# Optimization experiments

Hardware: AMD Instinct MI355X
Metric: run time of the kernel (lower is better)

The kernel has to match this reference:

```python
import jax, jax.numpy as jnp
import numpy as np

N = 100000
E = 1600000
D = 128


def setup_inputs() -> dict:
    key = jax.random.key(0)
    ks = jax.random.split(key, 9)
    s = 1.0 / np.sqrt(D)
    return {
        "x": jax.random.normal(ks[0], (N, D), dtype=jnp.float32),
        "edge_index": jax.random.randint(ks[1], (2, E), 0, N, dtype=jnp.int64),
        # SAGEConv layer 1: lin_l (neighbor path, with bias), lin_r (root path, no bias)
        "Wl1": jax.random.normal(ks[2], (D, D), dtype=jnp.float32) * s,
        "bl1": jnp.zeros((D,), dtype=jnp.float32),
        "Wr1": jax.random.normal(ks[3], (D, D), dtype=jnp.float32) * s,
        # SAGEConv layer 2
        "Wl2": jax.random.normal(ks[4], (D, D), dtype=jnp.float32) * s,
        "bl2": jnp.zeros((D,), dtype=jnp.float32),
        "Wr2": jax.random.normal(ks[5], (D, D), dtype=jnp.float32) * s,
    }


def _sage_conv(x, src, dst, Wl, bl, Wr):
    # PyG SAGEConv, aggr='mean', root_weight=True:
    #   out = lin_l(mean_{j in N(i)} x_j) + lin_r(x_i)
    msg = x[src]                                              # [E, D] gather
    agg = jax.ops.segment_sum(msg, dst, num_segments=N)       # [N, D]
    cnt = jax.ops.segment_sum(jnp.ones((src.shape[0],), x.dtype), dst, num_segments=N)
    agg = agg / jnp.maximum(cnt, 1.0)[:, None]                # mean aggregation
    return agg @ Wl.T + bl + x @ Wr.T


def reference(x, edge_index, Wl1, bl1, Wr1, Wl2, bl2, Wr2):
    src, dst = edge_index[0], edge_index[1]
    h = jax.nn.relu(_sage_conv(x, src, dst, Wl1, bl1, Wr1))
    out = _sage_conv(h, src, dst, Wl2, bl2, Wr2)
    return out
```

## Files before the change

### kernel.cpp

```cpp
#include <hip/hip_runtime.h>
#include <stdint.h>

#define DN 128
#define NBITS 6
#define BNODES 64
#define HB 2048
#define NSL 64
#define NLOC 256

__host__ __device__ static inline int divup(int a, int b){ return (a+b-1)/b; }

typedef __attribute__((ext_vector_type(8))) short bf16x8;
typedef __attribute__((ext_vector_type(4))) float floatx4;

__device__ __forceinline__ unsigned short f2bf(float f){
  unsigned int x = __float_as_uint(f);
  unsigned int r = x + 0x7fffu + ((x >> 16) & 1u);
  return (unsigned short)(r >> 16);
}
__device__ __forceinline__ unsigned int pack2(unsigned short a, unsigned short b){
  return (unsigned int)a | ((unsigned int)b << 16);
}


__global__ __launch_bounds__(256)
void hist_pass(const int* __restrict__ dst, int* __restrict__ gHist, int E){
  __shared__ int h[NLOC];
  int p = blockIdx.x & 7, s = blockIdx.x >> 3;
  int t = threadIdx.x;
  h[t] = 0;
  __syncthreads();
  int n4 = E >> 2, per4 = divup(n4, NSL);
  int lo = s*per4, hi = min(lo+per4, n4);
  const int4* dst4 = (const int4*)dst;
  for (int i = lo + t; i < hi; i += 256){
    int4 d4 = dst4[i];
    int dd[4] = {d4.x, d4.y, d4.z, d4.w};
    #pragma unroll
    for (int j=0;j<4;j++){
      int b = dd[j] >> NBITS;
      if ((b & 7) == p) atomicAdd(&h[b>>3], 1);
    }
  }
  if (s == NSL-1){
    for (int e = (n4<<2) + t; e < E; e += 256){
      int b = dst[e] >> NBITS;
      if ((b & 7) == p) atomicAdd(&h[b>>3], 1);
    }
  }
  __syncthreads();
  gHist[blockIdx.x*NLOC + t] = h[t];
}

__global__ __launch_bounds__(256)
void scan_offsets(const int* __restrict__ gHist, int* __restrict__ blockOffset,
                  int* __restrict__ bucketTotal){
  int b = blockIdx.x*4 + (threadIdx.x >> 6);
  int k = threadIdx.x & 63;
  int p = b & 7, lb = b >> 3;
  int idx = (k*8 + p)*NLOC + lb;
  int v = gHist[idx];
  int sft = v;
  #pragma unroll
  for (int off=1; off<64; off<<=1){
    int u = __shfl_up(sft, off, 64);
    if (k >= off) sft += u;
  }
  blockOffset[idx] = sft - v;
  if (k == 63) bucketTotal[b] = sft;
}

__global__ __launch_bounds__(256)
void bucket_base(const int* __restrict__ bucketTotal, int* __restrict__ bucketBase){
  __shared__ int s[256];
  int t = threadIdx.x;
  int v[8]; int sum = 0;
  #pragma unroll
  for (int j=0;j<8;j++){ v[j] = bucketTotal[t*8+j]; sum += v[j]; }
  s[t] = sum; __syncthreads();
  for (int off=1; off<256; off<<=1){
    int y = (t>=off)? s[t-off] : 0;
    __syncthreads();
    s[t] += y;
    __syncthreads();
  }
  int excl = s[t] - sum;
  #pragma unroll
  for (int j=0;j<8;j++){ bucketBase[t*8+j] = excl; excl += v[j]; }
  if (t == 255) bucketBase[HB] = excl;
}

__global__ __launch_bounds__(256)
void scatter_pass(const int* __restrict__ src, const int* __restrict__ dst,
                  const int* __restrict__ bucketBase, const int* __restrict__ blockOffset,
                  unsigned int* __restrict__ packed, int E){
  __shared__ int cur[NLOC];
  int p = blockIdx.x & 7, s = blockIdx.x >> 3;
  int t = threadIdx.x;
  cur[t] = bucketBase[(t<<3)|p] + blockOffset[blockIdx.x*NLOC + t];
  __syncthreads();
  int n4 = E >> 2, per4 = divup(n4, NSL);
  int lo = s*per4, hi = min(lo+per4, n4);
  const int4* dst4 = (const int4*)dst;
  const int4* src4 = (const int4*)src;
  for (int i = lo + t; i < hi; i += 256){
    int4 d4 = dst4[i];
    int4 s4 = src4[i];
    int dd[4] = {d4.x, d4.y, d4.z, d4.w};
    int ss[4] = {s4.x, s4.y, s4.z, s4.w};
    #pragma unroll
    for (int j=0;j<4;j++){
      int d = dd[j], b = d >> NBITS;
      if ((b & 7) == p){
        int pos = atomicAdd(&cur[b>>3], 1);
        packed[pos] = (unsigned)ss[j] | ((unsigned)(d & (BNODES-1)) << 17);
      }
    }
  }
  if (s == NSL-1){
    for (int e = (n4<<2) + t; e < E; e += 256){
      int d = dst[e], b = d >> NBITS;
      if ((b & 7) == p){
        int pos = atomicAdd(&cur[b>>3], 1);
        packed[pos] = (unsigned)src[e] | ((unsigned)(d & (BNODES-1)) << 17);
      }
    }
  }
}

__global__ __launch_bounds__(256)
void node_sort(const int* __restrict__ bucketBase, const unsigned int* __restrict__ packed,
               int* __restrict__ csr_src, int* __restrict__ nodeOff, int n){
  __shared__ int cnts[BNODES], offs[BNODES+1], cursor[BNODES];
  int b = blockIdx.x, t = threadIdx.x;
  int beg = bucketBase[b], end = bucketBase[b+1], cnt = end - beg;
  if (t < BNODES) cnts[t] = 0;
  __syncthreads();
  for (int i=t; i<cnt; i+=256) atomicAdd(&cnts[(packed[beg+i]>>17)&63], 1);
  __syncthreads();
  if (t < BNODES){
    int v = cnts[t], sft = v;
    #pragma unroll
    for (int off=1; off<64; off<<=1){
      int u = __shfl_up(sft, off, 64);
      if (t >= off) sft += u;
    }
    offs[t] = sft - v; cursor[t] = sft - v;
    if (t == 63) offs[BNODES] = sft;
  }
  __syncthreads();
  for (int i=t; i<cnt; i+=256){
    unsigned pk = packed[beg+i];
    int nd = (pk>>17)&63;
    int r = atomicAdd(&cursor[nd], 1);
    csr_src[beg + r] = (int)(pk & 0x1FFFFu);
  }
  if (t <= BNODES){
    int node = b*BNODES + t;
    if (node <= n) nodeOff[node] = beg + offs[t];
  }
}


__global__ __launch_bounds__(256)
void convert_x_kernel(const float* __restrict__ src, unsigned short* __restrict__ dst, int count8){
  int i = blockIdx.x*256 + threadIdx.x;
  if (i >= count8) return;
  const float4* s = (const float4*)src + (size_t)i*2;
  float4 a = s[0], b = s[1];
  uint4 o;
  o.x = pack2(f2bf(a.x), f2bf(a.y));
  o.y = pack2(f2bf(a.z), f2bf(a.w));
  o.z = pack2(f2bf(b.x), f2bf(b.y));
  o.w = pack2(f2bf(b.z), f2bf(b.w));
  ((uint4*)dst)[i] = o;
}

__global__ __launch_bounds__(256)
void convert_w_kernel(const float* __restrict__ w0, const float* __restrict__ w1,
                      const float* __restrict__ w2, const float* __restrict__ w3,
                      unsigned short* __restrict__ dst){
  int tid = blockIdx.x*256 + threadIdx.x;
  if (tid >= 8192) return;
  int mat = tid >> 11, off = tid & 2047;
  const float* w = (mat==0)?w0:(mat==1)?w1:(mat==2)?w2:w3;
  const float4* s = (const float4*)w + (size_t)off*2;
  float4 a = s[0], b = s[1];
  uint4 o;
  o.x = pack2(f2bf(a.x), f2bf(a.y));
  o.y = pack2(f2bf(a.z), f2bf(a.w));
  o.z = pack2(f2bf(b.x), f2bf(b.y));
  o.w = pack2(f2bf(b.z), f2bf(b.w));
  ((uint4*)(dst + (size_t)mat*16384))[off] = o;
}

__global__ __launch_bounds__(256)
void aggregate_csr(const unsigned short* __restrict__ xb, const int* __restrict__ nodeOff,
                   const int* __restrict__ csr_src, unsigned short* __restrict__ aggb, int n){
  int g = (blockIdx.x*256 + threadIdx.x) >> 6;
  if (g >= n) return;
  int lane = threadIdx.x & 63;
  int j = lane >> 4;
  int l = lane & 15;
  int beg = nodeOff[g], end = nodeOff[g+1];
  float acc[8] = {0,0,0,0,0,0,0,0};
  #define ACCUM(u) { unsigned int w;                                   \
      w=(u).x; acc[0]+=__uint_as_float(w<<16); acc[1]+=__uint_as_float(w&0xffff0000u); \
      w=(u).y; acc[2]+=__uint_as_float(w<<16); acc[3]+=__uint_as_float(w&0xffff0000u); \
      w=(u).z; acc[4]+=__uint_as_float(w<<16); acc[5]+=__uint_as_float(w&0xffff0000u); \
      w=(u).w; acc[6]+=__uint_as_float(w<<16); acc[7]+=__uint_as_float(w&0xffff0000u); }
  const uint4* x4 = (const uint4*)xb;
  int p = beg;
  for (; p + 8 <= end; p += 8){
    int s0 = csr_src[p + j];
    int s1 = csr_src[p + 4 + j];
    uint4 u0 = x4[(size_t)s0*16 + l];
    uint4 u1 = x4[(size_t)s1*16 + l];
    ACCUM(u0) ACCUM(u1)
  }
  for (; p + 4 <= end; p += 4){
    int s0 = csr_src[p + j];
    uint4 u0 = x4[(size_t)s0*16 + l];
    ACCUM(u0)
  }
  int rem = end - p;
  if (j < rem){
    int s0 = csr_src[p + j];
    uint4 u0 = x4[(size_t)s0*16 + l];
    ACCUM(u0)
  }
  #undef ACCUM
  #pragma unroll
  for (int k=0;k<8;k++){
    acc[k] += __shfl_xor(acc[k], 16, 64);
    acc[k] += __shfl_xor(acc[k], 32, 64);
  }
  if (j == 0){
    float inv = 1.f / fmaxf((float)(end-beg), 1.f);
    uint4 o;
    o.x = pack2(f2bf(acc[0]*inv), f2bf(acc[1]*inv));
    o.y = pack2(f2bf(acc[2]*inv), f2bf(acc[3]*inv));
    o.z = pack2(f2bf(acc[4]*inv), f2bf(acc[5]*inv));
    o.w = pack2(f2bf(acc[6]*inv), f2bf(acc[7]*inv));
    ((uint4*)(aggb + (size_t)g*DN))[l] = o;
  }
}

template<bool RELU, bool OUT_BF16>
__global__ __launch_bounds__(256)
void gemm_mfma(const unsigned short* __restrict__ A1, const unsigned short* __restrict__ W1b,
               const unsigned short* __restrict__ A2, const unsigned short* __restrict__ W2b,
               const float* __restrict__ bias, void* __restrict__ out,
               int rt_total, int rt_per_block)
{
  int wave = threadIdx.x >> 6;
  int lane = threadIdx.x & 63;
  int m = lane & 15, quad = lane >> 4;

  bf16x8 Bf[2][2][4];
  {
    const unsigned short* Ws[2] = {W1b, W2b};
    #pragma unroll
    for (int c2=0;c2<2;c2++){
      int col = wave*32 + c2*16 + m;
      #pragma unroll
      for (int mat=0;mat<2;mat++){
        const unsigned short* wrow = Ws[mat] + (size_t)col*DN + quad*8;
        #pragma unroll
        for (int kc=0;kc<4;kc++)
          Bf[c2][mat][kc] = *(const bf16x8*)(wrow + kc*32);
      }
    }
  }
  float bv0 = bias[wave*32 + m];
  float bv1 = bias[wave*32 + 16 + m];

  int rt_begin = blockIdx.x * rt_per_block;
  int rt_end = rt_begin + rt_per_block; if (rt_end > rt_total) rt_end = rt_total;

  for (int rt = rt_begin; rt < rt_end; ++rt){
    const unsigned short* a1p = A1 + ((size_t)(rt*16 + m))*DN + quad*8;
    const unsigned short* a2p = A2 + ((size_t)(rt*16 + m))*DN + quad*8;
    bf16x8 Af[2][4];
    #pragma unroll
    for (int kc=0;kc<4;kc++){
      Af[0][kc] = *(const bf16x8*)(a1p + kc*32);
      Af[1][kc] = *(const bf16x8*)(a2p + kc*32);
    }
    __syncthreads();
    floatx4 acc0 = {0.f,0.f,0.f,0.f}, acc1 = {0.f,0.f,0.f,0.f};
    #pragma unroll
    for (int mat=0; mat<2; mat++)
      #pragma unroll
      for (int kc=0; kc<4; kc++){
        acc0 = __builtin_amdgcn_mfma_f32_16x16x32_bf16(Af[mat][kc], Bf[0][mat][kc], acc0, 0,0,0);
        acc1 = __builtin_amdgcn_mfma_f32_16x16x32_bf16(Af[mat][kc], Bf[1][mat][kc], acc1, 0,0,0);
      }
    #pragma unroll
    for (int r=0;r<4;r++){
      int row = rt*16 + quad*4 + r;
      float v0 = acc0[r] + bv0;
      float v1 = acc1[r] + bv1;
      if (RELU){ v0 = fmaxf(v0, 0.f); v1 = fmaxf(v1, 0.f); }
      if (OUT_BF16){
        unsigned short* o = (unsigned short*)out + (size_t)row*DN + wave*32 + m;
        o[0]  = f2bf(v0);
        o[16] = f2bf(v1);
      } else {
        float* o = (float*)out + (size_t)row*DN + wave*32 + m;
        o[0]  = v0;
        o[16] = v1;
      }
    }
  }
}


extern "C" void kernel_launch(void* const* d_in, const int* in_sizes, int n_in,
                              void* d_out, int out_size, void* d_ws, size_t ws_size,
                              hipStream_t stream) {
  const float* x   = (const float*)d_in[0];
  const int*   ei  = (const int*)d_in[1];
  const float* Wl1 = (const float*)d_in[2];
  const float* bl1 = (const float*)d_in[3];
  const float* Wr1 = (const float*)d_in[4];
  const float* Wl2 = (const float*)d_in[5];
  const float* bl2 = (const float*)d_in[6];
  const float* Wr2 = (const float*)d_in[7];

  const int n = in_sizes[0] / DN;
  const int E = in_sizes[1] / 2;
  const int* src = ei;
  const int* dst = ei + E;

  char* ws = (char*)d_ws;
  char* ws_end = ws + ws_size;
  int* gHist       = (int*)ws;  ws += (size_t)NSL*8*NLOC*4;
  int* blockOffset = (int*)ws;  ws += (size_t)NSL*8*NLOC*4;
  int* bucketTotal = (int*)ws;  ws += (size_t)HB*4;
  int* bucketBase  = (int*)ws;  ws += (size_t)(HB+1)*4;
  ws = (char*)(((uintptr_t)ws + 255) & ~(uintptr_t)255);
  unsigned int* packed = (unsigned int*)ws; ws += (size_t)E*4;
  int* csr_src     = (int*)ws;  ws += (size_t)E*4;
  int* nodeOff     = (int*)ws;  ws += (size_t)(n+1)*4;
  ws = (char*)(((uintptr_t)ws + 255) & ~(uintptr_t)255);
  unsigned short* Wb   = (unsigned short*)ws; ws += 4*16384*2;
  unsigned short* xb   = (unsigned short*)ws; ws += (size_t)n*DN*2;
  unsigned short* aggb = (unsigned short*)ws; ws += (size_t)n*DN*2;
  unsigned short* hb = xb;
  if (ws + (size_t)n*DN*2 <= ws_end) { hb = (unsigned short*)ws; ws += (size_t)n*DN*2; }

  unsigned short* Wl1b = Wb;
  unsigned short* Wr1b = Wb + 16384;
  unsigned short* Wl2b = Wb + 2*16384;
  unsigned short* Wr2b = Wb + 3*16384;

  hist_pass   <<<NSL*8, 256,0,stream>>>(dst, gHist, E);
  scan_offsets<<<HB/4,  256,0,stream>>>(gHist, blockOffset, bucketTotal);
  bucket_base <<<1,     256,0,stream>>>(bucketTotal, bucketBase);
  scatter_pass<<<NSL*8, 256,0,stream>>>(src, dst, bucketBase, blockOffset, packed, E);
  node_sort   <<<HB,    256,0,stream>>>(bucketBase, packed, csr_src, nodeOff, n);

  convert_x_kernel<<<divup(n*DN/8,256),256,0,stream>>>(x, xb, n*DN/8);
  convert_w_kernel<<<32,256,0,stream>>>(Wl1, Wr1, Wl2, Wr2, Wb);

  const int rt_total = n / 16;
  const int rt_per_block = 5;
  const int gblocks = divup(rt_total, rt_per_block);
  const int agrid = divup(n*64, 256);

  aggregate_csr<<<agrid,256,0,stream>>>(xb, nodeOff, csr_src, aggb, n);
  gemm_mfma<true, true><<<gblocks,256,0,stream>>>(aggb, Wl1b, xb, Wr1b, bl1, hb, rt_total, rt_per_block);
  aggregate_csr<<<agrid,256,0,stream>>>(hb, nodeOff, csr_src, aggb, n);
  gemm_mfma<false,false><<<gblocks,256,0,stream>>>(aggb, Wl2b, hb, Wr2b, bl2, d_out, rt_total, rt_per_block);
}
```

Baseline: 365.0 us.

## Fuse mean aggregation and dual GEMM into one SAGE layer kernel

Adds a fused kernel per SAGE layer: each block gathers and mean-aggregates 32 nodes into shared memory as bf16, then runs MFMA against both Wl and Wr with bias and optional ReLU in the epilogue. This removes the round trip of the aggregated buffer through global memory and halves the per-layer kernel launches. In exchange, each block reloads both weight matrices into registers for only 32 rows, and the gather phase uses 16 lanes per node, which may cut memory-level parallelism compared with the separate aggregate kernel. The old path is kept as a fallback when the workspace cannot hold a separate h buffer.

```diff
diff --git a/kernel.cpp b/kernel.cpp
--- a/kernel.cpp
+++ b/kernel.cpp
@@ -193,6 +193,130 @@
   o.w = pack2(f2bf(b.z), f2bf(b.w));
   ((uint4*)(dst + (size_t)mat*16384))[off] = o;
 }
+
+template<bool RELU, bool OUT_BF16>
+__global__ __launch_bounds__(256, 4)
+void fused_sage(const unsigned short* __restrict__ xin, const int* __restrict__ nodeOff,
+                const int* __restrict__ csr_src,
+                const unsigned short* __restrict__ Wlb, const unsigned short* __restrict__ Wrb,
+                const float* __restrict__ bias, void* __restrict__ out, int n)
+{
+  __shared__ uint4 Asm[32][16];
+  int t = threadIdx.x;
+  int tile = blockIdx.x;
+  int nl = t >> 4;
+  int l  = t & 15;
+  const uint4* x4 = (const uint4*)xin;
+
+  #pragma unroll
+  for (int half = 0; half < 2; ++half){
+    int node_local = nl + half*16;
+    int g = tile*32 + node_local;
+    float acc[8] = {0,0,0,0,0,0,0,0};
+    int deg = 0;
+    if (g < n){
+      int beg = nodeOff[g], end = nodeOff[g+1];
+      deg = end - beg;
+      #define ACCUM(u) { unsigned int w;                                   \
+          w=(u).x; acc[0]+=__uint_as_float(w<<16); acc[1]+=__uint_as_float(w&0xffff0000u); \
+          w=(u).y; acc[2]+=__uint_as_float(w<<16); acc[3]+=__uint_as_float(w&0xffff0000u); \
+          w=(u).z; acc[4]+=__uint_as_float(w<<16); acc[5]+=__uint_as_float(w&0xffff0000u); \
+          w=(u).w; acc[6]+=__uint_as_float(w<<16); acc[7]+=__uint_as_float(w&0xffff0000u); }
+      int p = beg;
+      for (; p+4 <= end; p += 4){
+        int s0 = csr_src[p], s1 = csr_src[p+1], s2 = csr_src[p+2], s3 = csr_src[p+3];
+        uint4 u0 = x4[(size_t)s0*16 + l];
+        uint4 u1 = x4[(size_t)s1*16 + l];
+        uint4 u2 = x4[(size_t)s2*16 + l];
+        uint4 u3 = x4[(size_t)s3*16 + l];
+        ACCUM(u0) ACCUM(u1) ACCUM(u2) ACCUM(u3)
+      }
+      for (; p < end; ++p){
+        int s0 = csr_src[p];
+        uint4 u0 = x4[(size_t)s0*16 + l];
+        ACCUM(u0)
+      }
+      #undef ACCUM
+    }
+    float inv = 1.f / fmaxf((float)deg, 1.f);
+    uint4 o;
+    o.x = pack2(f2bf(acc[0]*inv), f2bf(acc[1]*inv));
+    o.y = pack2(f2bf(acc[2]*inv), f2bf(acc[3]*inv));
+    o.z = pack2(f2bf(acc[4]*inv), f2bf(acc[5]*inv));
+    o.w = pack2(f2bf(acc[6]*inv), f2bf(acc[7]*inv));
+    Asm[node_local][l ^ (node_local & 15)] = o;
+  }
+  __syncthreads();
+
+  int wave = t >> 6;
+  int lane = t & 63;
+  int m = lane & 15, quad = lane >> 4;
+
+  bf16x8 Bf[2][2][4];
+  {
+    const unsigned short* Ws[2] = {Wlb, Wrb};
+    #pragma unroll
+    for (int c2=0;c2<2;c2++){
+      int col = wave*32 + c2*16 + m;
+      #pragma unroll
+      for (int mat=0;mat<2;mat++){
+        const unsigned short* wrow = Ws[mat] + (size_t)col*DN + quad*8;
+        #pragma unroll
+        for (int kc=0;kc<4;kc++)
+          Bf[c2][mat][kc] = *(const bf16x8*)(wrow + kc*32);
+      }
+    }
+  }
+  float bv0 = bias[wave*32 + m];
+  float bv1 = bias[wave*32 + 16 + m];
+
+  #pragma unroll
+  for (int rt = 0; rt < 2; ++rt){
+    int arow = rt*16 + m;
+    int grow = tile*32 + arow;
+    bf16x8 Axf[4];
+    {
+      const unsigned short* xp = xin + (size_t)grow*DN + quad*8;
+      #pragma unroll
+      for (int kc=0;kc<4;kc++) Axf[kc] = *(const bf16x8*)(xp + kc*32);
+    }
+    bf16x8 Aaf[4];
+    #pragma unroll
+    for (int kc=0;kc<4;kc++){
+      int c = (quad + kc*4) ^ m;
+      Aaf[kc] = *(const bf16x8*)&Asm[arow][c];
+    }
+    floatx4 acc0 = {0.f,0.f,0.f,0.f}, acc1 = {0.f,0.f,0.f,0.f};
+    #pragma unroll
+    for (int kc=0; kc<4; kc++){
+      acc0 = __builtin_amdgcn_mfma_f32_16x16x32_bf16(Aaf[kc], Bf[0][0][kc], acc0, 0,0,0);
+      acc1 = __builtin_amdgcn_mfma_f32_16x16x32_bf16(Aaf[kc], Bf[1][0][kc], acc1, 0,0,0);
+    }
+    #pragma unroll
+    for (int kc=0; kc<4; kc++){
+      acc0 = __builtin_amdgcn_mfma_f32_16x16x32_bf16(Axf[kc], Bf[0][1][kc], acc0, 0,0,0);
+      acc1 = __builtin_amdgcn_mfma_f32_16x16x32_bf16(Axf[kc], Bf[1][1][kc], acc1, 0,0,0);
+    }
+    #pragma unroll
+    for (int r=0;r<4;r++){
+      int row = tile*32 + rt*16 + quad*4 + r;
+      if (row >= n) continue;
+      float v0 = acc0[r] + bv0;
+      float v1 = acc1[r] + bv1;
+      if (RELU){ v0 = fmaxf(v0, 0.f); v1 = fmaxf(v1, 0.f); }
+      if (OUT_BF16){
+        unsigned short* o = (unsigned short*)out + (size_t)row*DN + wave*32 + m;
+        o[0]  = f2bf(v0);
+        o[16] = f2bf(v1);
+      } else {
+        float* o = (float*)out + (size_t)row*DN + wave*32 + m;
+        o[0]  = v0;
+        o[16] = v1;
+      }
+    }
+  }
+}
+
 
 __global__ __launch_bounds__(256)
 void aggregate_csr(const unsigned short* __restrict__ xb, const int* __restrict__ nodeOff,
@@ -348,7 +472,8 @@
   unsigned short* xb   = (unsigned short*)ws; ws += (size_t)n*DN*2;
   unsigned short* aggb = (unsigned short*)ws; ws += (size_t)n*DN*2;
   unsigned short* hb = xb;
-  if (ws + (size_t)n*DN*2 <= ws_end) { hb = (unsigned short*)ws; ws += (size_t)n*DN*2; }
+  bool have_hb = false;
+  if (ws + (size_t)n*DN*2 <= ws_end) { hb = (unsigned short*)ws; ws += (size_t)n*DN*2; have_hb = true; }
 
   unsigned short* Wl1b = Wb;
   unsigned short* Wr1b = Wb + 16384;
@@ -364,13 +489,18 @@
   convert_x_kernel<<<divup(n*DN/8,256),256,0,stream>>>(x, xb, n*DN/8);
   convert_w_kernel<<<32,256,0,stream>>>(Wl1, Wr1, Wl2, Wr2, Wb);
 
-  const int rt_total = n / 16;
-  const int rt_per_block = 5;
-  const int gblocks = divup(rt_total, rt_per_block);
-  const int agrid = divup(n*64, 256);
-
-  aggregate_csr<<<agrid,256,0,stream>>>(xb, nodeOff, csr_src, aggb, n);
-  gemm_mfma<true, true><<<gblocks,256,0,stream>>>(aggb, Wl1b, xb, Wr1b, bl1, hb, rt_total, rt_per_block);
-  aggregate_csr<<<agrid,256,0,stream>>>(hb, nodeOff, csr_src, aggb, n);
-  gemm_mfma<false,false><<<gblocks,256,0,stream>>>(aggb, Wl2b, hb, Wr2b, bl2, d_out, rt_total, rt_per_block);
-}
+  if (have_hb){
+    const int ftiles = divup(n, 32);
+    fused_sage<true, true ><<<ftiles,256,0,stream>>>(xb, nodeOff, csr_src, Wl1b, Wr1b, bl1, hb,    n);
+    fused_sage<false,false><<<ftiles,256,0,stream>>>(hb, nodeOff, csr_src, Wl2b, Wr2b, bl2, d_out, n);
+  } else {
+    const int rt_total = n / 16;
+    const int rt_per_block = 5;
+    const int gblocks = divup(rt_total, rt_per_block);
+    const int agrid = divup(n*64, 256);
+    aggregate_csr<<<agrid,256,0,stream>>>(xb, nodeOff, csr_src, aggb, n);
+    gemm_mfma<true, true ><<<gblocks,256,0,stream>>>(aggb, Wl1b, xb, Wr1b, bl1, hb, rt_total, rt_per_block);
+    aggregate_csr<<<agrid,256,0,stream>>>(hb, nodeOff, csr_src, aggb, n);
+    gemm_mfma<false,false><<<gblocks,256,0,stream>>>(aggb, Wl2b, hb, Wr2b, bl2, d_out, rt_total, rt_per_block);
+  }
+}
```

New measurement: 369.5 us. About the same (+1.2%).
